# Kernel optimization log

Hardware: AMD Instinct MI355X
Metric: run time of the kernel (lower is better)

Reference implementation:

```python
import jax, jax.numpy as jnp
import numpy as np

N_EDGE_TYPES = 25
EF = 2  # edge feature dim (excluding type)
HID = 10


def _edge_nn(et, ef, emb, wh, bh, wg, bg):
    # y = relu(emb[et] * (ef@Wh+bh) + (ef@Wg+bg)) -> [E, in*out]
    return jax.nn.relu(emb[et] * (ef @ wh + bh) + (ef @ wg + bg))


def _nnconv(x, et, ef, src, dst, emb, wh, bh, wg, bg, root, bias, in_c, out_c):
    n = x.shape[0]
    w = _edge_nn(et, ef, emb, wh, bh, wg, bg).reshape(-1, in_c, out_c)  # [E,in,out]
    msg = jnp.einsum('ei,eio->eo', x[src], w)                          # per-edge matmul
    s = jax.ops.segment_sum(msg, dst, num_segments=n)
    cnt = jax.ops.segment_sum(jnp.ones((src.shape[0],), x.dtype), dst, num_segments=n)
    agg = s / jnp.maximum(cnt, 1.0)[:, None]                           # scatter-mean
    return agg + x @ root + bias


def _make_params(key, in_c, out_c):
    ks = jax.random.split(key, 6)
    d = in_c * out_c
    s = 0.1
    return dict(
        emb=jax.random.normal(ks[0], (N_EDGE_TYPES, d), jnp.float32) * s,
        wh=jax.random.normal(ks[1], (EF, d), jnp.float32) * s,
        bh=jax.random.normal(ks[2], (d,), jnp.float32) * s,
        wg=jax.random.normal(ks[3], (EF, d), jnp.float32) * s,
        bg=jax.random.normal(ks[4], (d,), jnp.float32) * s,
        root=jax.random.normal(ks[5], (in_c, out_c), jnp.float32) * s,
        bias=jnp.zeros((out_c,), jnp.float32),
    )


def setup_inputs() -> dict:
    key = jax.random.key(0)
    ks = jax.random.split(key, 12)
    N, E, IN_C, OUT_C, B = 50000, 250000, 16, 16, 8
    inp = {
        'x': jax.random.normal(ks[0], (N, IN_C), jnp.float32),
        'edge_feat': jax.random.normal(ks[1], (E, EF), jnp.float32),
        'edge_type': jax.random.randint(ks[2], (E,), 0, N_EDGE_TYPES),
        'edge_src': jax.random.randint(ks[3], (E,), 0, N),
        'edge_dst': jax.random.randint(ks[4], (E,), 0, N),
        'cell_type': jax.random.randint(ks[5], (N,), 0, 3),
        'batch_ids': jnp.sort(jax.random.randint(ks[6], (N,), 0, B)),
        'batch_size': B,
    }
    for i, (ic, oc) in enumerate([(IN_C, HID), (HID, HID), (HID, OUT_C)], start=1):
        p = _make_params(ks[6 + i], ic, oc)
        for k, v in p.items():
            inp[f'{k}{i}'] = v
    return inp


def reference(x, edge_feat,
              emb1, wh1, bh1, wg1, bg1, root1, bias1,
              emb2, wh2, bh2, wg2, bg2, root2, bias2,
              emb3, wh3, bh3, wg3, bg3, root3, bias3,
              edge_type, edge_src, edge_dst, cell_type, batch_ids, batch_size):
    in_c, out_c = x.shape[1], root3.shape[1]
    h = _nnconv(x, edge_type, edge_feat, edge_src, edge_dst,
                emb1, wh1, bh1, wg1, bg1, root1, bias1, in_c, HID)
    h = jax.nn.relu(h)  # dropout is identity in eval mode
    h = _nnconv(h, edge_type, edge_feat, edge_src, edge_dst,
                emb2, wh2, bh2, wg2, bg2, root2, bias2, HID, HID)
    h = jax.nn.relu(h)
    h = _nnconv(h, edge_type, edge_feat, edge_src, edge_dst,
                emb3, wh3, bh3, wg3, bg3, root3, bias3, HID, out_c)
    h = jax.nn.relu(h)
    # scatter-mean pooling over nodes with cell_type==1, grouped by graph id
    gate = (cell_type == 1).astype(jnp.int32)
    idx = gate * (batch_ids.astype(jnp.int32) + 1)  # 0 = discarded bucket
    nseg = batch_size + 1
    s = jax.ops.segment_sum(h, idx, num_segments=nseg)
    cnt = jax.ops.segment_sum(jnp.ones((h.shape[0],), h.dtype), idx, num_segments=nseg)
    pooled = s / jnp.maximum(cnt, 1.0)[:, None]
    return pooled[1:batch_size + 1, :]  # [B, out_c]
```

## Files before the change

### kernel.cpp

```cpp
#include <hip/hip_runtime.h>
#include <stdint.h>

#define IN1 16
#define HIDC 10
#define OUT3 16
#define NTYPES 25
#define MAXB 32

__global__ __launch_bounds__(256) void zero2_kernel(int* __restrict__ a, int na,
                                                    int* __restrict__ b, int nb) {
  int i = blockIdx.x * blockDim.x + threadIdx.x;
  int s = gridDim.x * blockDim.x;
  for (int j = i; j < na; j += s) a[j] = 0;
  for (int j = i; j < nb; j += s) b[j] = 0;
}

__global__ __launch_bounds__(256) void hist_kernel(const int* __restrict__ edst,
                                                   int* __restrict__ deg,
                                                   int* __restrict__ pos, int E) {
  int e = blockIdx.x * blockDim.x + threadIdx.x;
  if (e < E) pos[e] = atomicAdd(&deg[edst[e]], 1);
}

__global__ __launch_bounds__(256) void scan_part_kernel(const int* __restrict__ deg,
                                                        int* __restrict__ row_ptr,
                                                        int* __restrict__ bsum, int N) {
  __shared__ int wsums[4];
  int tid = threadIdx.x, lane = tid & 63, wid = tid >> 6;
  int idx0 = (blockIdx.x * 256 + tid) * 4;
  int4 v = make_int4(0, 0, 0, 0);
  if (idx0 < N)     v.x = deg[idx0];
  if (idx0 + 1 < N) v.y = deg[idx0 + 1];
  if (idx0 + 2 < N) v.z = deg[idx0 + 2];
  if (idx0 + 3 < N) v.w = deg[idx0 + 3];
  int s = v.x + v.y + v.z + v.w;
  int x = s;
  #pragma unroll
  for (int off = 1; off < 64; off <<= 1) {
    int y = __shfl_up(x, off);
    if (lane >= off) x += y;
  }
  if (lane == 63) wsums[wid] = x;
  __syncthreads();
  int wpre = 0;
  #pragma unroll
  for (int w = 0; w < 4; ++w) if (w < wid) wpre += wsums[w];
  int excl = x - s + wpre;
  if (idx0 < N)     row_ptr[idx0]     = excl;
  if (idx0 + 1 < N) row_ptr[idx0 + 1] = excl + v.x;
  if (idx0 + 2 < N) row_ptr[idx0 + 2] = excl + v.x + v.y;
  if (idx0 + 3 < N) row_ptr[idx0 + 3] = excl + v.x + v.y + v.z;
  if (tid == 255) bsum[blockIdx.x] = excl + s;
}

__global__ __launch_bounds__(64) void scan_bsum_kernel(int* __restrict__ bsum,
                                                       int* __restrict__ row_ptr,
                                                       int G, int N) {
  int tid = threadIdx.x;
  int v = (tid < G) ? bsum[tid] : 0;
  int x = v;
  #pragma unroll
  for (int off = 1; off < 64; off <<= 1) {
    int y = __shfl_up(x, off);
    if (tid >= off) x += y;
  }
  if (tid < G) bsum[tid] = x - v;
  if (tid == 63) row_ptr[N] = x;
}

__global__ __launch_bounds__(256) void scan_add_kernel(int* __restrict__ row_ptr,
                                                       const int* __restrict__ bsum,
                                                       int N) {
  int i = blockIdx.x * blockDim.x + threadIdx.x;
  if (i < N) row_ptr[i] += bsum[i >> 10];
}

__global__ __launch_bounds__(256) void permute_kernel(
    const int* __restrict__ edst, const int* __restrict__ esrc,
    const int* __restrict__ et, const float2* __restrict__ ef,
    const int* __restrict__ row_ptr, const int* __restrict__ pos,
    int4* __restrict__ edges, int E) {
  int e = blockIdx.x * blockDim.x + threadIdx.x;
  if (e >= E) return;
  int d = edst[e];
  int idx = row_ptr[d] + pos[e];
  float2 f = ef[e];
  int4 r;
  r.x = esrc[e];
  r.y = et[e];
  r.z = __float_as_int(f.x);
  r.w = __float_as_int(f.y);
  edges[idx] = r;
}

template<int IN_C, int O, bool POOL, int BS>
__global__ __launch_bounds__(BS) void layer_kernel(
    const float* __restrict__ xin,
    const int4* __restrict__ edges,
    const int* __restrict__ row_ptr,
    const float* __restrict__ emb,
    const float* __restrict__ wh, const float* __restrict__ bh,
    const float* __restrict__ wg, const float* __restrict__ bg,
    const float* __restrict__ root,
    const float* __restrict__ bias,
    float* __restrict__ hout,
    const int* __restrict__ ctype, const int* __restrict__ bids,
    float* __restrict__ pcnt,
    int N, int B)
{
  constexpr int D = IN_C * O;
  constexpr int ESTR = D + 8;
  constexpr int NPB = BS / 16;
  __shared__ float4 s_pa[D];
  __shared__ float2 s_pb[D];
  __shared__ float s_emb[NTYPES * ESTR];
  __shared__ float s_root[D];
  __shared__ float s_bias[O];
  __shared__ float s_psum[POOL ? (MAXB * 16) : 1];
  __shared__ float s_pcnt[POOL ? MAXB : 1];

  int tid = threadIdx.x;
  for (int k = tid; k < D; k += BS) {
    s_pa[k] = make_float4(wh[k], wh[D + k], wg[k], wg[D + k]);
    s_pb[k] = make_float2(bh[k], bg[k]);
    s_root[k] = root[k];
  }
  for (int k = tid; k < NTYPES * D; k += BS) {
    int t = k / D, j = k - t * D;
    s_emb[t * ESTR + j] = emb[k];
  }
  if (tid < O) s_bias[tid] = bias[tid];
  if (POOL) {
    for (int i = tid; i < MAXB * 16; i += BS) s_psum[i] = 0.f;
    for (int i = tid; i < MAXB; i += BS) s_pcnt[i] = 0.f;
  }
  __syncthreads();

  int nl = tid >> 4;
  int o = tid & 15;
  int oc = (O == 16) ? o : ((o < O) ? o : 0);
  int n = blockIdx.x * NPB + nl;

  float acc = 0.f;
  int start = 0, end = 0;
  if (n < N) { start = row_ptr[n]; end = row_ptr[n + 1]; }
  for (int e = start; e < end; ++e) {
    int4 r = edges[e];
    int src = r.x, t = r.y;
    float f0 = __int_as_float(r.z), f1 = __int_as_float(r.w);
    const float* __restrict__ xr = xin + (size_t)src * IN_C;
    const float* __restrict__ er = s_emb + t * ESTR;
    #pragma unroll
    for (int i = 0; i < IN_C; ++i) {
      int k = i * O + oc;
      float4 a = s_pa[k];
      float2 b = s_pb[k];
      float h = fmaf(f0, a.x, fmaf(f1, a.y, b.x));
      float g = fmaf(f0, a.z, fmaf(f1, a.w, b.y));
      float w = fmaxf(fmaf(er[k], h, g), 0.f);
      acc = fmaf(xr[i], w, acc);
    }
  }

  if (n < N && o < O) {
    float inv = 1.0f / fmaxf((float)(end - start), 1.0f);
    float v = fmaf(acc, inv, s_bias[o]);
    const float* __restrict__ xr = xin + (size_t)n * IN_C;
    #pragma unroll
    for (int i = 0; i < IN_C; ++i) v = fmaf(xr[i], s_root[i * O + o], v);
    v = fmaxf(v, 0.f);
    if (!POOL) {
      hout[(size_t)n * O + o] = v;
    } else {
      if (ctype[n] == 1) {
        int b = bids[n];
        atomicAdd(&s_psum[b * 16 + o], v);
        if (o == 0) atomicAdd(&s_pcnt[b], 1.0f);
      }
    }
  }

  if (POOL) {
    __syncthreads();
    for (int i = tid; i < B * 16; i += BS) {
      float v = s_psum[i];
      if (v != 0.f) atomicAdd(&hout[i], v);
    }
    for (int i = tid; i < B; i += BS) {
      float c = s_pcnt[i];
      if (c != 0.f) atomicAdd(&pcnt[i], c);
    }
  }
}

__global__ __launch_bounds__(256) void finalize_kernel(
    const float* __restrict__ psum, const float* __restrict__ pcnt,
    float* __restrict__ out, int B) {
  int i = blockIdx.x * blockDim.x + threadIdx.x;
  if (i >= B * OUT3) return;
  int b = i / OUT3;
  out[i] = psum[i] / fmaxf(pcnt[b], 1.0f);
}

extern "C" void kernel_launch(void* const* d_in, const int* in_sizes, int n_in,
                              void* d_out, int out_size, void* d_ws, size_t ws_size,
                              hipStream_t stream)
{
  const float* x     = (const float*)d_in[0];
  const float* ef    = (const float*)d_in[1];
  const int*   et    = (const int*)d_in[2];
  const int*   esrc  = (const int*)d_in[3];
  const int*   edst  = (const int*)d_in[4];
  const int*   ctype = (const int*)d_in[5];
  const int*   bids  = (const int*)d_in[6];
  const float* emb1 = (const float*)d_in[8];
  const float* wh1  = (const float*)d_in[9];
  const float* bh1  = (const float*)d_in[10];
  const float* wg1  = (const float*)d_in[11];
  const float* bg1  = (const float*)d_in[12];
  const float* root1= (const float*)d_in[13];
  const float* bias1= (const float*)d_in[14];
  const float* emb2 = (const float*)d_in[15];
  const float* wh2  = (const float*)d_in[16];
  const float* bh2  = (const float*)d_in[17];
  const float* wg2  = (const float*)d_in[18];
  const float* bg2  = (const float*)d_in[19];
  const float* root2= (const float*)d_in[20];
  const float* bias2= (const float*)d_in[21];
  const float* emb3 = (const float*)d_in[22];
  const float* wh3  = (const float*)d_in[23];
  const float* bh3  = (const float*)d_in[24];
  const float* wg3  = (const float*)d_in[25];
  const float* bg3  = (const float*)d_in[26];
  const float* root3= (const float*)d_in[27];
  const float* bias3= (const float*)d_in[28];

  const int N = in_sizes[0] / IN1;
  const int E = in_sizes[2];
  const int B = out_size / OUT3;

  int4* edges   = (int4*)d_ws;
  int*  deg     = (int*)(edges + E);
  int*  pos     = deg + N;
  int*  row_ptr = pos + E;
  int*  bsum    = row_ptr + (N + 1);
  float* h1     = (float*)(bsum + 64);
  float* h2     = h1 + (size_t)N * HIDC;
  float* psum   = h2 + (size_t)N * HIDC;
  float* pcnt   = psum + (size_t)B * 16;

  const int nChunk = (N + 1023) / 1024;

  zero2_kernel<<<128, 256, 0, stream>>>(deg, N, (int*)psum, B * 16 + B);
  hist_kernel<<<(E + 255) / 256, 256, 0, stream>>>(edst, deg, pos, E);
  scan_part_kernel<<<nChunk, 256, 0, stream>>>(deg, row_ptr, bsum, N);
  scan_bsum_kernel<<<1, 64, 0, stream>>>(bsum, row_ptr, nChunk, N);
  scan_add_kernel<<<(N + 255) / 256, 256, 0, stream>>>(row_ptr, bsum, N);
  permute_kernel<<<(E + 255) / 256, 256, 0, stream>>>(
      edst, esrc, et, (const float2*)ef, row_ptr, pos, edges, E);

  const int g256 = (N + 15) / 16;
  layer_kernel<IN1, HIDC, false, 256><<<g256, 256, 0, stream>>>(
      x, edges, row_ptr, emb1, wh1, bh1, wg1, bg1, root1, bias1,
      h1, nullptr, nullptr, nullptr, N, B);
  layer_kernel<HIDC, HIDC, false, 256><<<g256, 256, 0, stream>>>(
      h1, edges, row_ptr, emb2, wh2, bh2, wg2, bg2, root2, bias2,
      h2, nullptr, nullptr, nullptr, N, B);

  const int g1024 = (N + 63) / 64;
  layer_kernel<HIDC, OUT3, true, 1024><<<g1024, 1024, 0, stream>>>(
      h2, edges, row_ptr, emb3, wh3, bh3, wg3, bg3, root3, bias3,
      psum, ctype, bids, pcnt, N, B);

  finalize_kernel<<<1, 256, 0, stream>>>(psum, pcnt, (float*)d_out, B);
}
```

Before: 257.9 us.

## Use persistent grid-stride blocks in layer kernels and vectorize embedding staging

Layer kernels now launch a fixed-size persistent grid (1024 or 512 blocks). Each wavefront loops over groups of 4 nodes in grid-stride fashion instead of one block per 16 nodes. This amortizes the per-block shared-memory staging of emb/weights over many nodes, which had been repeated across ~3000 blocks. Embedding staging also uses float4 loads and stores. The risk is lower occupancy or load imbalance from the fixed grid size.

```diff
diff --git a/kernel.cpp b/kernel.cpp
--- a/kernel.cpp
+++ b/kernel.cpp
@@ -110,10 +110,12 @@
 {
   constexpr int D = IN_C * O;
   constexpr int ESTR = D + 8;
-  constexpr int NPB = BS / 16;
+  static_assert(ESTR % 4 == 0, "ESTR must keep float4 alignment");
+  static_assert((NTYPES * D) % 4 == 0, "emb size must be float4-divisible");
+  static_assert(D % 4 == 0, "emb row must be float4-divisible");
   __shared__ float4 s_pa[D];
   __shared__ float2 s_pb[D];
-  __shared__ float s_emb[NTYPES * ESTR];
+  __shared__ __align__(16) float s_emb[NTYPES * ESTR];
   __shared__ float s_root[D];
   __shared__ float s_bias[O];
   __shared__ float s_psum[POOL ? (MAXB * 16) : 1];
@@ -125,9 +127,13 @@
     s_pb[k] = make_float2(bh[k], bg[k]);
     s_root[k] = root[k];
   }
-  for (int k = tid; k < NTYPES * D; k += BS) {
+  const float4* __restrict__ emb4 = (const float4*)emb;
+  constexpr int T4 = NTYPES * D / 4;
+  for (int k4 = tid; k4 < T4; k4 += BS) {
+    float4 v = emb4[k4];
+    int k = k4 * 4;
     int t = k / D, j = k - t * D;
-    s_emb[t * ESTR + j] = emb[k];
+    *(float4*)&s_emb[t * ESTR + j] = v;
   }
   if (tid < O) s_bias[tid] = bias[tid];
   if (POOL) {
@@ -136,46 +142,51 @@
   }
   __syncthreads();
 
-  int nl = tid >> 4;
   int o = tid & 15;
+  int sub = (tid >> 4) & 3;
   int oc = (O == 16) ? o : ((o < O) ? o : 0);
-  int n = blockIdx.x * NPB + nl;
-
-  float acc = 0.f;
-  int start = 0, end = 0;
-  if (n < N) { start = row_ptr[n]; end = row_ptr[n + 1]; }
-  for (int e = start; e < end; ++e) {
-    int4 r = edges[e];
-    int src = r.x, t = r.y;
-    float f0 = __int_as_float(r.z), f1 = __int_as_float(r.w);
-    const float* __restrict__ xr = xin + (size_t)src * IN_C;
-    const float* __restrict__ er = s_emb + t * ESTR;
-    #pragma unroll
-    for (int i = 0; i < IN_C; ++i) {
-      int k = i * O + oc;
-      float4 a = s_pa[k];
-      float2 b = s_pb[k];
-      float h = fmaf(f0, a.x, fmaf(f1, a.y, b.x));
-      float g = fmaf(f0, a.z, fmaf(f1, a.w, b.y));
-      float w = fmaxf(fmaf(er[k], h, g), 0.f);
-      acc = fmaf(xr[i], w, acc);
-    }
-  }
-
-  if (n < N && o < O) {
-    float inv = 1.0f / fmaxf((float)(end - start), 1.0f);
-    float v = fmaf(acc, inv, s_bias[o]);
-    const float* __restrict__ xr = xin + (size_t)n * IN_C;
-    #pragma unroll
-    for (int i = 0; i < IN_C; ++i) v = fmaf(xr[i], s_root[i * O + o], v);
-    v = fmaxf(v, 0.f);
-    if (!POOL) {
-      hout[(size_t)n * O + o] = v;
-    } else {
-      if (ctype[n] == 1) {
-        int b = bids[n];
-        atomicAdd(&s_psum[b * 16 + o], v);
-        if (o == 0) atomicAdd(&s_pcnt[b], 1.0f);
+  int gw = blockIdx.x * (BS / 64) + (tid >> 6);
+  int nw = gridDim.x * (BS / 64);
+  int nWT = (N + 3) >> 2;
+
+  for (int wt = gw; wt < nWT; wt += nw) {
+    int n = wt * 4 + sub;
+    float acc = 0.f;
+    int start = 0, end = 0;
+    if (n < N) { start = row_ptr[n]; end = row_ptr[n + 1]; }
+    for (int e = start; e < end; ++e) {
+      int4 r = edges[e];
+      int src = r.x, t = r.y;
+      float f0 = __int_as_float(r.z), f1 = __int_as_float(r.w);
+      const float* __restrict__ xr = xin + (size_t)src * IN_C;
+      const float* __restrict__ er = s_emb + t * ESTR;
+      #pragma unroll
+      for (int i = 0; i < IN_C; ++i) {
+        int k = i * O + oc;
+        float4 a = s_pa[k];
+        float2 b = s_pb[k];
+        float h = fmaf(f0, a.x, fmaf(f1, a.y, b.x));
+        float g = fmaf(f0, a.z, fmaf(f1, a.w, b.y));
+        float w = fmaxf(fmaf(er[k], h, g), 0.f);
+        acc = fmaf(xr[i], w, acc);
+      }
+    }
+
+    if (n < N && o < O) {
+      float inv = 1.0f / fmaxf((float)(end - start), 1.0f);
+      float v = fmaf(acc, inv, s_bias[o]);
+      const float* __restrict__ xr = xin + (size_t)n * IN_C;
+      #pragma unroll
+      for (int i = 0; i < IN_C; ++i) v = fmaf(xr[i], s_root[i * O + o], v);
+      v = fmaxf(v, 0.f);
+      if (!POOL) {
+        hout[(size_t)n * O + o] = v;
+      } else {
+        if (ctype[n] == 1) {
+          int b = bids[n];
+          atomicAdd(&s_psum[b * 16 + o], v);
+          if (o == 0) atomicAdd(&s_pcnt[b], 1.0f);
+        }
       }
     }
   }
@@ -259,16 +270,16 @@
   permute_kernel<<<(E + 255) / 256, 256, 0, stream>>>(
       edst, esrc, et, (const float2*)ef, row_ptr, pos, edges, E);
 
-  const int g256 = (N + 15) / 16;
-  layer_kernel<IN1, HIDC, false, 256><<<g256, 256, 0, stream>>>(
+  const int gP = 1024;
+  layer_kernel<IN1, HIDC, false, 256><<<gP, 256, 0, stream>>>(
       x, edges, row_ptr, emb1, wh1, bh1, wg1, bg1, root1, bias1,
       h1, nullptr, nullptr, nullptr, N, B);
-  layer_kernel<HIDC, HIDC, false, 256><<<g256, 256, 0, stream>>>(
+  layer_kernel<HIDC, HIDC, false, 256><<<gP, 256, 0, stream>>>(
       h1, edges, row_ptr, emb2, wh2, bh2, wg2, bg2, root2, bias2,
       h2, nullptr, nullptr, nullptr, N, B);
 
-  const int g1024 = (N + 63) / 64;
-  layer_kernel<HIDC, OUT3, true, 1024><<<g1024, 1024, 0, stream>>>(
+  const int gQ = 512;
+  layer_kernel<HIDC, OUT3, true, 1024><<<gQ, 1024, 0, stream>>>(
       h2, edges, row_ptr, emb3, wh3, bh3, wg3, bg3, root3, bias3,
       psum, ctype, bids, pcnt, N, B);
 
```

Result: slower. 272.1 us (+5.5%).

## Vectorize gathers with padded hidden rows, register-resident edge-NN weights

Applied to the files above, without the earlier changes.

Hidden activations are stored with a padded row stride of 12 so per-edge source rows can be loaded with float4/float2 vector loads. The embedding table in shared memory is transposed to [type][out][in] with padding so each thread reads its embedding column with vector LDS loads. The edge-NN linear weights and biases are kept in per-thread registers instead of being read from shared memory on every edge. This cuts scalar global and LDS load instructions in the inner edge loop, but raises register pressure (six arrays of IN_C floats) and may lower occupancy, especially for the 16-input layer.

```diff
diff --git a/kernel.cpp b/kernel.cpp
--- a/kernel.cpp
+++ b/kernel.cpp
@@ -6,6 +6,7 @@
 #define OUT3 16
 #define NTYPES 25
 #define MAXB 32
+#define HSTR 12
 
 __global__ __launch_bounds__(256) void zero2_kernel(int* __restrict__ a, int na,
                                                     int* __restrict__ b, int nb) {
@@ -93,7 +94,7 @@
   edges[idx] = r;
 }
 
-template<int IN_C, int O, bool POOL, int BS>
+template<int IN_C, int O, int XS, bool POOL, int BS>
 __global__ __launch_bounds__(BS) void layer_kernel(
     const float* __restrict__ xin,
     const int4* __restrict__ edges,
@@ -109,26 +110,23 @@
     int N, int B)
 {
   constexpr int D = IN_C * O;
-  constexpr int ESTR = D + 8;
+  constexpr int ISTR = (IN_C + 3) & ~3;
+  constexpr int ISTRP = (ISTR == IN_C) ? (ISTR + 4) : ISTR;
+  constexpr int TSTR = O * ISTRP;
   constexpr int NPB = BS / 16;
-  __shared__ float4 s_pa[D];
-  __shared__ float2 s_pb[D];
-  __shared__ float s_emb[NTYPES * ESTR];
+  __shared__ __align__(16) float s_emb[NTYPES * TSTR];
   __shared__ float s_root[D];
   __shared__ float s_bias[O];
   __shared__ float s_psum[POOL ? (MAXB * 16) : 1];
   __shared__ float s_pcnt[POOL ? MAXB : 1];
 
   int tid = threadIdx.x;
-  for (int k = tid; k < D; k += BS) {
-    s_pa[k] = make_float4(wh[k], wh[D + k], wg[k], wg[D + k]);
-    s_pb[k] = make_float2(bh[k], bg[k]);
-    s_root[k] = root[k];
-  }
   for (int k = tid; k < NTYPES * D; k += BS) {
-    int t = k / D, j = k - t * D;
-    s_emb[t * ESTR + j] = emb[k];
-  }
+    int t = k / D, r = k - t * D;
+    int i = r / O, ocq = r - i * O;
+    s_emb[t * TSTR + ocq * ISTRP + i] = emb[k];
+  }
+  for (int k = tid; k < D; k += BS) s_root[k] = root[k];
   if (tid < O) s_bias[tid] = bias[tid];
   if (POOL) {
     for (int i = tid; i < MAXB * 16; i += BS) s_psum[i] = 0.f;
@@ -140,6 +138,14 @@
   int o = tid & 15;
   int oc = (O == 16) ? o : ((o < O) ? o : 0);
   int n = blockIdx.x * NPB + nl;
+
+  float cwh0[IN_C], cwh1[IN_C], cbh[IN_C], cwg0[IN_C], cwg1[IN_C], cbg[IN_C];
+  #pragma unroll
+  for (int i = 0; i < IN_C; ++i) {
+    int k = i * O + oc;
+    cwh0[i] = wh[k]; cwh1[i] = wh[D + k]; cbh[i] = bh[k];
+    cwg0[i] = wg[k]; cwg1[i] = wg[D + k]; cbg[i] = bg[k];
+  }
 
   float acc = 0.f;
   int start = 0, end = 0;
@@ -148,29 +154,48 @@
     int4 r = edges[e];
     int src = r.x, t = r.y;
     float f0 = __int_as_float(r.z), f1 = __int_as_float(r.w);
-    const float* __restrict__ xr = xin + (size_t)src * IN_C;
-    const float* __restrict__ er = s_emb + t * ESTR;
+    float xv[IN_C];
+    const float* __restrict__ xr = xin + (size_t)src * XS;
+    #pragma unroll
+    for (int q = 0; q < IN_C / 4; ++q) {
+      float4 v = ((const float4*)xr)[q];
+      xv[4 * q + 0] = v.x; xv[4 * q + 1] = v.y;
+      xv[4 * q + 2] = v.z; xv[4 * q + 3] = v.w;
+    }
+    if constexpr (IN_C % 4 == 2) {
+      float2 v = ((const float2*)xr)[IN_C / 2 - 1];
+      xv[IN_C - 2] = v.x; xv[IN_C - 1] = v.y;
+    }
+    const float* __restrict__ er = s_emb + t * TSTR + oc * ISTRP;
+    float ev[IN_C];
+    #pragma unroll
+    for (int q = 0; q < IN_C / 4; ++q) {
+      float4 v = ((const float4*)er)[q];
+      ev[4 * q + 0] = v.x; ev[4 * q + 1] = v.y;
+      ev[4 * q + 2] = v.z; ev[4 * q + 3] = v.w;
+    }
+    if constexpr (IN_C % 4 == 2) {
+      float2 v = ((const float2*)er)[IN_C / 2 - 1];
+      ev[IN_C - 2] = v.x; ev[IN_C - 1] = v.y;
+    }
     #pragma unroll
     for (int i = 0; i < IN_C; ++i) {
-      int k = i * O + oc;
-      float4 a = s_pa[k];
-      float2 b = s_pb[k];
-      float h = fmaf(f0, a.x, fmaf(f1, a.y, b.x));
-      float g = fmaf(f0, a.z, fmaf(f1, a.w, b.y));
-      float w = fmaxf(fmaf(er[k], h, g), 0.f);
-      acc = fmaf(xr[i], w, acc);
+      float h = fmaf(f0, cwh0[i], fmaf(f1, cwh1[i], cbh[i]));
+      float g = fmaf(f0, cwg0[i], fmaf(f1, cwg1[i], cbg[i]));
+      float w = fmaxf(fmaf(ev[i], h, g), 0.f);
+      acc = fmaf(xv[i], w, acc);
     }
   }
 
   if (n < N && o < O) {
     float inv = 1.0f / fmaxf((float)(end - start), 1.0f);
     float v = fmaf(acc, inv, s_bias[o]);
-    const float* __restrict__ xr = xin + (size_t)n * IN_C;
+    const float* __restrict__ xr = xin + (size_t)n * XS;
     #pragma unroll
     for (int i = 0; i < IN_C; ++i) v = fmaf(xr[i], s_root[i * O + o], v);
     v = fmaxf(v, 0.f);
     if (!POOL) {
-      hout[(size_t)n * O + o] = v;
+      hout[(size_t)n * HSTR + o] = v;
     } else {
       if (ctype[n] == 1) {
         int b = bids[n];
@@ -245,8 +270,8 @@
   int*  row_ptr = pos + E;
   int*  bsum    = row_ptr + (N + 1);
   float* h1     = (float*)(bsum + 64);
-  float* h2     = h1 + (size_t)N * HIDC;
-  float* psum   = h2 + (size_t)N * HIDC;
+  float* h2     = h1 + (size_t)N * HSTR;
+  float* psum   = h2 + (size_t)N * HSTR;
   float* pcnt   = psum + (size_t)B * 16;
 
   const int nChunk = (N + 1023) / 1024;
@@ -260,15 +285,15 @@
       edst, esrc, et, (const float2*)ef, row_ptr, pos, edges, E);
 
   const int g256 = (N + 15) / 16;
-  layer_kernel<IN1, HIDC, false, 256><<<g256, 256, 0, stream>>>(
+  layer_kernel<IN1, HIDC, IN1, false, 256><<<g256, 256, 0, stream>>>(
       x, edges, row_ptr, emb1, wh1, bh1, wg1, bg1, root1, bias1,
       h1, nullptr, nullptr, nullptr, N, B);
-  layer_kernel<HIDC, HIDC, false, 256><<<g256, 256, 0, stream>>>(
+  layer_kernel<HIDC, HIDC, HSTR, false, 256><<<g256, 256, 0, stream>>>(
       h1, edges, row_ptr, emb2, wh2, bh2, wg2, bg2, root2, bias2,
       h2, nullptr, nullptr, nullptr, N, B);
 
   const int g1024 = (N + 63) / 64;
-  layer_kernel<HIDC, OUT3, true, 1024><<<g1024, 1024, 0, stream>>>(
+  layer_kernel<HIDC, OUT3, HSTR, true, 1024><<<g1024, 1024, 0, stream>>>(
       h2, edges, row_ptr, emb3, wh3, bh3, wg3, bg3, root3, bias3,
       psum, ctype, bids, pcnt, N, B);
 
```

Result: slower. 309.8 us (+20.1%).

## Precompute per-type edge-net coefficients and vectorize gathered node features

Applied to the files above, without the earlier changes.

Adds a prep kernel that folds emb, wh, bh, wg and bg into one float4 per (type, weight) entry, so each edge weight becomes relu(f0*a+f1*b+c). Each layer stages this table in shared memory and reads node features as float4/float2 from a row stride padded to 12, cutting per-edge FMAs and shared loads. Hidden layers move to 512-thread blocks, root and bias are read straight from global memory, and MAXB drops to 8. The per-block shared table is larger (up to 25*160 float4, about 64KB), which may lower occupancy, and MAXB 8 assumes batch_size is at most 8.

```diff
diff --git a/kernel.cpp b/kernel.cpp
--- a/kernel.cpp
+++ b/kernel.cpp
@@ -5,7 +5,12 @@
 #define HIDC 10
 #define OUT3 16
 #define NTYPES 25
-#define MAXB 32
+#define MAXB 8
+#define HSTR 12
+
+#define D1 (IN1 * HIDC)
+#define D2 (HIDC * HIDC)
+#define D3 (HIDC * OUT3)
 
 __global__ __launch_bounds__(256) void zero2_kernel(int* __restrict__ a, int na,
                                                     int* __restrict__ b, int nb) {
@@ -93,14 +98,46 @@
   edges[idx] = r;
 }
 
-template<int IN_C, int O, bool POOL, int BS>
+__global__ __launch_bounds__(256) void prep_kernel(
+    const float* __restrict__ emb1, const float* __restrict__ wh1,
+    const float* __restrict__ bh1, const float* __restrict__ wg1,
+    const float* __restrict__ bg1,
+    const float* __restrict__ emb2, const float* __restrict__ wh2,
+    const float* __restrict__ bh2, const float* __restrict__ wg2,
+    const float* __restrict__ bg2,
+    const float* __restrict__ emb3, const float* __restrict__ wh3,
+    const float* __restrict__ bh3, const float* __restrict__ wg3,
+    const float* __restrict__ bg3,
+    float4* __restrict__ P1, float4* __restrict__ P2, float4* __restrict__ P3)
+{
+  int i = blockIdx.x * 256 + threadIdx.x;
+  const float *emb, *wh, *bh, *wg, *bg;
+  float4* P; int D, k;
+  if (i < NTYPES * D1) {
+    emb = emb1; wh = wh1; bh = bh1; wg = wg1; bg = bg1; P = P1; D = D1; k = i;
+  } else if (i < NTYPES * (D1 + D2)) {
+    emb = emb2; wh = wh2; bh = bh2; wg = wg2; bg = bg2; P = P2; D = D2;
+    k = i - NTYPES * D1;
+  } else if (i < NTYPES * (D1 + D2 + D3)) {
+    emb = emb3; wh = wh3; bh = bh3; wg = wg3; bg = bg3; P = P3; D = D3;
+    k = i - NTYPES * (D1 + D2);
+  } else return;
+  int j = k - (k / D) * D;
+  float e = emb[k];
+  float4 p;
+  p.x = fmaf(e, wh[j],     wg[j]);
+  p.y = fmaf(e, wh[D + j], wg[D + j]);
+  p.z = fmaf(e, bh[j],     bg[j]);
+  p.w = 0.f;
+  P[k] = p;
+}
+
+template<int IN_C, int O, int XS, bool POOL, int BS>
 __global__ __launch_bounds__(BS) void layer_kernel(
     const float* __restrict__ xin,
     const int4* __restrict__ edges,
     const int* __restrict__ row_ptr,
-    const float* __restrict__ emb,
-    const float* __restrict__ wh, const float* __restrict__ bh,
-    const float* __restrict__ wg, const float* __restrict__ bg,
+    const float4* __restrict__ Pg,
     const float* __restrict__ root,
     const float* __restrict__ bias,
     float* __restrict__ hout,
@@ -109,27 +146,13 @@
     int N, int B)
 {
   constexpr int D = IN_C * O;
-  constexpr int ESTR = D + 8;
   constexpr int NPB = BS / 16;
-  __shared__ float4 s_pa[D];
-  __shared__ float2 s_pb[D];
-  __shared__ float s_emb[NTYPES * ESTR];
-  __shared__ float s_root[D];
-  __shared__ float s_bias[O];
+  __shared__ float4 s_P[NTYPES * D];
   __shared__ float s_psum[POOL ? (MAXB * 16) : 1];
   __shared__ float s_pcnt[POOL ? MAXB : 1];
 
   int tid = threadIdx.x;
-  for (int k = tid; k < D; k += BS) {
-    s_pa[k] = make_float4(wh[k], wh[D + k], wg[k], wg[D + k]);
-    s_pb[k] = make_float2(bh[k], bg[k]);
-    s_root[k] = root[k];
-  }
-  for (int k = tid; k < NTYPES * D; k += BS) {
-    int t = k / D, j = k - t * D;
-    s_emb[t * ESTR + j] = emb[k];
-  }
-  if (tid < O) s_bias[tid] = bias[tid];
+  for (int k = tid; k < NTYPES * D; k += BS) s_P[k] = Pg[k];
   if (POOL) {
     for (int i = tid; i < MAXB * 16; i += BS) s_psum[i] = 0.f;
     for (int i = tid; i < MAXB; i += BS) s_pcnt[i] = 0.f;
@@ -146,31 +169,39 @@
   if (n < N) { start = row_ptr[n]; end = row_ptr[n + 1]; }
   for (int e = start; e < end; ++e) {
     int4 r = edges[e];
-    int src = r.x, t = r.y;
     float f0 = __int_as_float(r.z), f1 = __int_as_float(r.w);
-    const float* __restrict__ xr = xin + (size_t)src * IN_C;
-    const float* __restrict__ er = s_emb + t * ESTR;
+    const float4* __restrict__ pb = s_P + r.y * D + oc;
+    const float* __restrict__ xr = xin + (size_t)r.x * XS;
     #pragma unroll
-    for (int i = 0; i < IN_C; ++i) {
-      int k = i * O + oc;
-      float4 a = s_pa[k];
-      float2 b = s_pb[k];
-      float h = fmaf(f0, a.x, fmaf(f1, a.y, b.x));
-      float g = fmaf(f0, a.z, fmaf(f1, a.w, b.y));
-      float w = fmaxf(fmaf(er[k], h, g), 0.f);
-      acc = fmaf(xr[i], w, acc);
+    for (int q = 0; q < IN_C / 4; ++q) {
+      float4 xq = ((const float4*)xr)[q];
+      float4 p0 = pb[(4 * q + 0) * O];
+      float4 p1 = pb[(4 * q + 1) * O];
+      float4 p2 = pb[(4 * q + 2) * O];
+      float4 p3 = pb[(4 * q + 3) * O];
+      acc = fmaf(xq.x, fmaxf(fmaf(f0, p0.x, fmaf(f1, p0.y, p0.z)), 0.f), acc);
+      acc = fmaf(xq.y, fmaxf(fmaf(f0, p1.x, fmaf(f1, p1.y, p1.z)), 0.f), acc);
+      acc = fmaf(xq.z, fmaxf(fmaf(f0, p2.x, fmaf(f1, p2.y, p2.z)), 0.f), acc);
+      acc = fmaf(xq.w, fmaxf(fmaf(f0, p3.x, fmaf(f1, p3.y, p3.z)), 0.f), acc);
+    }
+    if constexpr (IN_C % 4 == 2) {
+      float2 xq = ((const float2*)xr)[IN_C / 2 - 1];
+      float4 p0 = pb[(IN_C - 2) * O];
+      float4 p1 = pb[(IN_C - 1) * O];
+      acc = fmaf(xq.x, fmaxf(fmaf(f0, p0.x, fmaf(f1, p0.y, p0.z)), 0.f), acc);
+      acc = fmaf(xq.y, fmaxf(fmaf(f0, p1.x, fmaf(f1, p1.y, p1.z)), 0.f), acc);
     }
   }
 
   if (n < N && o < O) {
     float inv = 1.0f / fmaxf((float)(end - start), 1.0f);
-    float v = fmaf(acc, inv, s_bias[o]);
-    const float* __restrict__ xr = xin + (size_t)n * IN_C;
+    float v = fmaf(acc, inv, bias[o]);
+    const float* __restrict__ xr = xin + (size_t)n * XS;
     #pragma unroll
-    for (int i = 0; i < IN_C; ++i) v = fmaf(xr[i], s_root[i * O + o], v);
+    for (int i = 0; i < IN_C; ++i) v = fmaf(xr[i], root[i * O + o], v);
     v = fmaxf(v, 0.f);
     if (!POOL) {
-      hout[(size_t)n * O + o] = v;
+      hout[(size_t)n * HSTR + o] = v;
     } else {
       if (ctype[n] == 1) {
         int b = bids[n];
@@ -244,14 +275,22 @@
   int*  pos     = deg + N;
   int*  row_ptr = pos + E;
   int*  bsum    = row_ptr + (N + 1);
-  float* h1     = (float*)(bsum + 64);
-  float* h2     = h1 + (size_t)N * HIDC;
-  float* psum   = h2 + (size_t)N * HIDC;
+  uintptr_t pp  = ((uintptr_t)(bsum + 64) + 15) & ~(uintptr_t)15;
+  float4* P1    = (float4*)pp;
+  float4* P2    = P1 + NTYPES * D1;
+  float4* P3    = P2 + NTYPES * D2;
+  float* h1     = (float*)(P3 + NTYPES * D3);
+  float* h2     = h1 + (size_t)N * HSTR;
+  float* psum   = h2 + (size_t)N * HSTR;
   float* pcnt   = psum + (size_t)B * 16;
 
   const int nChunk = (N + 1023) / 1024;
+  const int nPrep  = NTYPES * (D1 + D2 + D3);
 
   zero2_kernel<<<128, 256, 0, stream>>>(deg, N, (int*)psum, B * 16 + B);
+  prep_kernel<<<(nPrep + 255) / 256, 256, 0, stream>>>(
+      emb1, wh1, bh1, wg1, bg1, emb2, wh2, bh2, wg2, bg2,
+      emb3, wh3, bh3, wg3, bg3, P1, P2, P3);
   hist_kernel<<<(E + 255) / 256, 256, 0, stream>>>(edst, deg, pos, E);
   scan_part_kernel<<<nChunk, 256, 0, stream>>>(deg, row_ptr, bsum, N);
   scan_bsum_kernel<<<1, 64, 0, stream>>>(bsum, row_ptr, nChunk, N);
@@ -259,17 +298,17 @@
   permute_kernel<<<(E + 255) / 256, 256, 0, stream>>>(
       edst, esrc, et, (const float2*)ef, row_ptr, pos, edges, E);
 
-  const int g256 = (N + 15) / 16;
-  layer_kernel<IN1, HIDC, false, 256><<<g256, 256, 0, stream>>>(
-      x, edges, row_ptr, emb1, wh1, bh1, wg1, bg1, root1, bias1,
+  const int g512 = (N + 31) / 32;
+  layer_kernel<IN1, HIDC, IN1, false, 512><<<g512, 512, 0, stream>>>(
+      x, edges, row_ptr, P1, root1, bias1,
       h1, nullptr, nullptr, nullptr, N, B);
-  layer_kernel<HIDC, HIDC, false, 256><<<g256, 256, 0, stream>>>(
-      h1, edges, row_ptr, emb2, wh2, bh2, wg2, bg2, root2, bias2,
+  layer_kernel<HIDC, HIDC, HSTR, false, 512><<<g512, 512, 0, stream>>>(
+      h1, edges, row_ptr, P2, root2, bias2,
       h2, nullptr, nullptr, nullptr, N, B);
 
   const int g1024 = (N + 63) / 64;
-  layer_kernel<HIDC, OUT3, true, 1024><<<g1024, 1024, 0, stream>>>(
-      h2, edges, row_ptr, emb3, wh3, bh3, wg3, bg3, root3, bias3,
+  layer_kernel<HIDC, OUT3, HSTR, true, 1024><<<g1024, 1024, 0, stream>>>(
+      h2, edges, row_ptr, P3, root3, bias3,
       psum, ctype, bids, pcnt, N, B);
 
   finalize_kernel<<<1, 256, 0, stream>>>(psum, pcnt, (float*)d_out, B);
```

New measurement: 251.2 us. 1.03x faster.
